# Optimization experiments

Measured on AMD Instinct MI355X. Metric: run time of the kernel, lower is better.

## Reference

```python
import jax, jax.numpy as jnp
import numpy as np

B, S, D = 4, 2048, 1024
H, DK, DV = 16, 64, 64
FF = 4096
EPS = 1e-6


def _ln(x, g, b):
    mu = jnp.mean(x, axis=-1, keepdims=True)
    var = jnp.mean((x - mu) ** 2, axis=-1, keepdims=True)
    return (x - mu) * jax.lax.rsqrt(var + EPS) * g + b


def setup_inputs() -> dict:
    key = jax.random.key(0)
    ks = jax.random.split(key, 12)
    sd = 0.02
    return {
        "src": jax.random.normal(ks[0], (B, S, D), jnp.float32),
        "attn_mask": jnp.zeros((B, S, S), jnp.bool_),
        "Wq": jax.random.normal(ks[1], (D, H * DK), jnp.float32) * sd,
        "bq": jnp.zeros((H * DK,), jnp.float32),
        "Wk": jax.random.normal(ks[2], (D, H * DK), jnp.float32) * sd,
        "bk": jnp.zeros((H * DK,), jnp.float32),
        "Wv": jax.random.normal(ks[3], (D, H * DV), jnp.float32) * sd,
        "bv": jnp.zeros((H * DV,), jnp.float32),
        "Wo": jax.random.normal(ks[4], (D, D), jnp.float32) * sd,
        "bo": jnp.zeros((D,), jnp.float32),
        "ln1_g": jnp.ones((D,), jnp.float32),
        "ln1_b": jnp.zeros((D,), jnp.float32),
        "W1": jax.random.normal(ks[5], (D, FF), jnp.float32) * sd,
        "b1": jnp.zeros((FF,), jnp.float32),
        "W2": jax.random.normal(ks[6], (FF, D), jnp.float32) * sd,
        "b2": jnp.zeros((D,), jnp.float32),
        "ln2_g": jnp.ones((D,), jnp.float32),
        "ln2_b": jnp.zeros((D,), jnp.float32),
    }


def reference(src, attn_mask, Wq, bq, Wk, bk, Wv, bv, Wo, bo,
              ln1_g, ln1_b, W1, b1, W2, b2, ln2_g, ln2_b):
    # QKV projections, split heads: [B,S,H*dk] -> [B,H,S,dk]
    q = (src @ Wq + bq).reshape(B, S, H, DK).transpose(0, 2, 1, 3)
    k = (src @ Wk + bk).reshape(B, S, H, DK).transpose(0, 2, 1, 3)
    v = (src @ Wv + bv).reshape(B, S, H, DV).transpose(0, 2, 1, 3)

    scale = 1.0 / (DK ** 0.5)
    scores = jnp.einsum("bhqd,bhkd->bhqk", q, k) * scale
    scores = jnp.where(attn_mask[:, None, :, :], -1e9, scores)
    attn = jax.nn.softmax(scores, axis=-1)  # dropout = identity (eval)
    ctx = jnp.einsum("bhqk,bhkd->bhqd", attn, v)
    ctx = ctx.transpose(0, 2, 1, 3).reshape(B, S, D)

    att_out = ctx @ Wo + bo  # dropout = identity (eval)
    x = _ln(src + att_out, ln1_g, ln1_b)

    h = jax.nn.relu(x @ W1 + b1)  # dropout = identity (eval)
    ffn_out = h @ W2 + b2
    return _ln(ffn_out + x, ln2_g, ln2_b)
```

## Files before the change

kernel.cpp:

```cpp
#include <hip/hip_runtime.h>
#include <stdint.h>

#define BB 4
#define SS 2048
#define DMODEL 1024
#define NH 16
#define FF 4096
#define MROWS (BB*SS)

typedef __bf16 bf16x8 __attribute__((ext_vector_type(8)));
typedef __bf16 bf16x2t __attribute__((ext_vector_type(2)));
typedef float f32x4 __attribute__((ext_vector_type(4)));
typedef float f32x16 __attribute__((ext_vector_type(16)));
typedef unsigned uintx4 __attribute__((ext_vector_type(4)));

__device__ __forceinline__ unsigned short f2b(float f) {
  unsigned u = __float_as_uint(f);
  unsigned r = (u + 0x7FFFu + ((u >> 16) & 1u)) >> 16;
  return (unsigned short)r;
}

__device__ __forceinline__ unsigned pack2bf(float a, float b) {
  bf16x2t v = {(__bf16)a, (__bf16)b};
  return __builtin_bit_cast(unsigned, v);
}

__device__ __forceinline__ void pls32(unsigned& x, unsigned& y) {
#if defined(__has_builtin) && __has_builtin(__builtin_amdgcn_permlane32_swap)
  auto r = __builtin_amdgcn_permlane32_swap(x, y, 0, 0);
  x = (unsigned)r[0];
  y = (unsigned)r[1];
#else
  const unsigned sx = (unsigned)__shfl_xor((int)x, 32, 64);
  const unsigned sy = (unsigned)__shfl_xor((int)y, 32, 64);
  const bool hi = ((threadIdx.x >> 5) & 1) != 0;
  const unsigned nx = hi ? sy : x;
  const unsigned ny = hi ? y : sx;
  x = nx; y = ny;
#endif
}

__device__ __forceinline__ void gload_lds16(const void* g, void* l) {
  __builtin_amdgcn_global_load_lds(
      (const __attribute__((address_space(1))) void*)g,
      (__attribute__((address_space(3))) void*)l, 16, 0, 0);
}

__device__ __forceinline__ bf16x8 lds_frag(const unsigned short* base, int row, int k) {
  unsigned off = (unsigned)((row * 128 + k * 2) ^ ((row & 7) << 4));
  return *reinterpret_cast<const bf16x8*>(reinterpret_cast<const char*>(base) + off);
}

__device__ __forceinline__ bf16x8 frag_rot(const unsigned short* base, int row, int kElem) {
  const int cb = kElem * 2;
  const unsigned off = (unsigned)(row * 128 + ((((cb >> 4) + row) & 7) << 4) + (cb & 15));
  return *reinterpret_cast<const bf16x8*>(reinterpret_cast<const char*>(base) + off);
}

__global__ __launch_bounds__(256) void f32_to_bf16_k(const float* __restrict__ in,
                                                     unsigned short* __restrict__ out, int n8) {
  const int i = blockIdx.x * 256 + threadIdx.x;
  if (i >= n8) return;
  const float4* p = reinterpret_cast<const float4*>(in) + (size_t)i * 2;
  const float4 a = p[0], c = p[1];
  uint4 o;
  o.x = (unsigned)f2b(a.x) | ((unsigned)f2b(a.y) << 16);
  o.y = (unsigned)f2b(a.z) | ((unsigned)f2b(a.w) << 16);
  o.z = (unsigned)f2b(c.x) | ((unsigned)f2b(c.y) << 16);
  o.w = (unsigned)f2b(c.z) | ((unsigned)f2b(c.w) << 16);
  reinterpret_cast<uint4*>(out)[i] = o;
}

__global__ __launch_bounds__(256) void transpose_convert4_k(
    const float* __restrict__ i0, const float* __restrict__ i1,
    const float* __restrict__ i2, const float* __restrict__ i3,
    unsigned short* __restrict__ o0, unsigned short* __restrict__ o1,
    unsigned short* __restrict__ o2, unsigned short* __restrict__ o3) {
  __shared__ float tile[32][33];
  const int z = blockIdx.z;
  const float* in = (z == 0) ? i0 : (z == 1) ? i1 : (z == 2) ? i2 : i3;
  unsigned short* out = (z == 0) ? o0 : (z == 1) ? o1 : (z == 2) ? o2 : o3;
  const int c0 = blockIdx.x * 32, r0 = blockIdx.y * 32;
  const int tx = threadIdx.x, ty = threadIdx.y;
  #pragma unroll
  for (int i = 0; i < 4; ++i)
    tile[ty + i * 8][tx] = in[(size_t)(r0 + ty + i * 8) * 1024 + c0 + tx];
  __syncthreads();
  #pragma unroll
  for (int i = 0; i < 4; ++i)
    out[(size_t)(c0 + ty + i * 8) * 1024 + r0 + tx] = f2b(tile[tx][ty + i * 8]);
}

__global__ __launch_bounds__(256) void transpose_convert_k(const float* __restrict__ in,
                                                           unsigned short* __restrict__ out,
                                                           int R, int C) {
  __shared__ float tile[32][33];
  const int c0 = blockIdx.x * 32, r0 = blockIdx.y * 32;
  const int tx = threadIdx.x, ty = threadIdx.y;
  #pragma unroll
  for (int i = 0; i < 4; ++i)
    tile[ty + i * 8][tx] = in[(size_t)(r0 + ty + i * 8) * C + c0 + tx];
  __syncthreads();
  #pragma unroll
  for (int i = 0; i < 4; ++i)
    out[(size_t)(c0 + ty + i * 8) * R + r0 + tx] = f2b(tile[tx][ty + i * 8]);
}

__global__ __launch_bounds__(256) void v_transpose_k(const unsigned short* __restrict__ Vb,
                                                     unsigned short* __restrict__ Vt) {
  __shared__ unsigned short tile[32][33];
  const int bh = blockIdx.z, b = bh >> 4, h = bh & 15;
  const int s0 = blockIdx.x * 32, d0 = blockIdx.y * 32;
  const int tx = threadIdx.x, ty = threadIdx.y;
  #pragma unroll
  for (int i = 0; i < 4; ++i)
    tile[ty + i * 8][tx] = Vb[(size_t)(b * SS + s0 + ty + i * 8) * DMODEL + h * 64 + d0 + tx];
  __syncthreads();
  #pragma unroll
  for (int i = 0; i < 4; ++i)
    Vt[(size_t)(bh * 64 + d0 + ty + i * 8) * SS + s0 + tx] = tile[tx][ty + i * 8];
}

__global__ __launch_bounds__(256) void mask_pack_k(const unsigned char* __restrict__ mask,
                                                   unsigned long long* __restrict__ mbits, int total) {
  const int idx = blockIdx.x * 256 + threadIdx.x;
  if (idx >= total) return;
  const uint4* p = reinterpret_cast<const uint4*>(mask) + (size_t)idx * 4;
  unsigned long long bits = 0ull;
  #pragma unroll
  for (int q = 0; q < 4; ++q) {
    uint4 v = p[q];
    unsigned wds[4] = {v.x, v.y, v.z, v.w};
    #pragma unroll
    for (int j = 0; j < 4; ++j)
      #pragma unroll
      for (int by = 0; by < 4; ++by)
        if ((wds[j] >> (by * 8)) & 0xFFu) bits |= 1ull << (q * 16 + j * 4 + by);
  }
  mbits[idx] = bits;
}

#define CQ 0.18033688011112042f
template <int EPI>
__global__ __launch_bounds__(256, 2) void gemm2_k(const unsigned short* __restrict__ A,
                                                  const unsigned short* __restrict__ Bt,
                                                  const float* __restrict__ bias_a,
                                                  const float* __restrict__ bias_b,
                                                  const float* __restrict__ bias_c,
                                                  void* __restrict__ Cout, int N, int K) {
  __shared__ __align__(16) unsigned short As[2][128 * 64];
  __shared__ __align__(16) unsigned short Bs[2][128 * 64];
  const int t = threadIdx.x;
  const int lane = t & 63, w = t >> 6;
  const int wr = w >> 1, wc = w & 1;
  const int lr = lane & 15, lg = lane >> 4;

  const int nwg = gridDim.x;
  const int q8 = nwg >> 3;
  const int wg = (blockIdx.x & 7) * q8 + (blockIdx.x >> 3);
  const int mb = wg & 63, nb = wg >> 6;
  const int m0 = mb * 128, n0 = nb * 128;

  const int srow = t >> 3;
  const unsigned cxor = (unsigned)(((t & 7) * 16) ^ (((t >> 3) & 7) << 4));
  const char* Asrc = reinterpret_cast<const char*>(A) + ((size_t)(m0 + srow) * K) * 2 + cxor;
  const char* Bsrc = reinterpret_cast<const char*>(Bt) + ((size_t)(n0 + srow) * K) * 2 + cxor;
  const size_t rstep = (size_t)32 * K * 2;
  char* AsB[2] = {reinterpret_cast<char*>(As[0]) + w * 1024, reinterpret_cast<char*>(As[1]) + w * 1024};
  char* BsB[2] = {reinterpret_cast<char*>(Bs[0]) + w * 1024, reinterpret_cast<char*>(Bs[1]) + w * 1024};

  auto stage = [&](int buf, int kt) {
    const char* ak = Asrc + (size_t)kt * 128;
    const char* bk = Bsrc + (size_t)kt * 128;
    #pragma unroll
    for (int c = 0; c < 4; ++c) {
      gload_lds16(ak + c * rstep, AsB[buf] + c * 4096);
      gload_lds16(bk + c * rstep, BsB[buf] + c * 4096);
    }
  };

  f32x4 acc[4][4] = {};
  const int nt = K >> 6;

  stage(0, 0);
  stage(1, 1);
  asm volatile("s_waitcnt vmcnt(8)" ::: "memory");
  __builtin_amdgcn_s_barrier();

  int cur = 0;
  for (int kt = 0; kt < nt; ++kt) {
    bf16x8 af[2][4], bfr[2][4];
    #pragma unroll
    for (int kk = 0; kk < 2; ++kk) {
      #pragma unroll
      for (int m = 0; m < 4; ++m)
        af[kk][m] = lds_frag(As[cur], wr * 64 + m * 16 + lr, kk * 32 + lg * 8);
      #pragma unroll
      for (int n = 0; n < 4; ++n)
        bfr[kk][n] = lds_frag(Bs[cur], wc * 64 + n * 16 + lr, kk * 32 + lg * 8);
    }
    __builtin_amdgcn_s_setprio(1);
    #pragma unroll
    for (int m = 0; m < 4; ++m)
      #pragma unroll
      for (int n = 0; n < 4; ++n)
        acc[m][n] = __builtin_amdgcn_mfma_f32_16x16x32_bf16(af[0][m], bfr[0][n], acc[m][n], 0, 0, 0);
    __builtin_amdgcn_s_setprio(0);

    asm volatile("s_waitcnt lgkmcnt(0)" ::: "memory");
    __builtin_amdgcn_s_barrier();
    if (kt + 2 < nt) {
      stage(cur, kt + 2);
      asm volatile("s_waitcnt vmcnt(8)" ::: "memory");
    } else {
      asm volatile("s_waitcnt vmcnt(0)" ::: "memory");
    }
    __builtin_amdgcn_s_barrier();
    __builtin_amdgcn_sched_barrier(0);

    __builtin_amdgcn_s_setprio(1);
    #pragma unroll
    for (int m = 0; m < 4; ++m)
      #pragma unroll
      for (int n = 0; n < 4; ++n)
        acc[m][n] = __builtin_amdgcn_mfma_f32_16x16x32_bf16(af[1][m], bfr[1][n], acc[m][n], 0, 0, 0);
    __builtin_amdgcn_s_setprio(0);
    cur ^= 1;
  }

  const int ccol0 = wc * 64;
  if constexpr (EPI == 3) {
    const int g3 = n0 >> 10;
    const float* bias = (g3 == 0) ? bias_a : (g3 == 1) ? bias_b : bias_c;
    const float scl = (g3 == 0) ? CQ : 1.0f;
    unsigned short* Og = reinterpret_cast<unsigned short*>(Cout) + (size_t)g3 * MROWS * DMODEL;
    const int ncol0 = (n0 & 1023) + ccol0;
    float bv[4];
    #pragma unroll
    for (int n = 0; n < 4; ++n) bv[n] = bias[ncol0 + n * 16 + lr];
    #pragma unroll
    for (int m = 0; m < 4; ++m)
      #pragma unroll
      for (int n = 0; n < 4; ++n)
        #pragma unroll
        for (int i = 0; i < 4; ++i) {
          const float v = (acc[m][n][i] + bv[n]) * scl;
          const size_t row = (size_t)(m0 + wr * 64 + m * 16 + lg * 4 + i);
          Og[row * DMODEL + (ncol0 + n * 16 + lr)] = f2b(v);
        }
  } else {
    float bv[4];
    #pragma unroll
    for (int n = 0; n < 4; ++n) bv[n] = bias_a[n0 + ccol0 + n * 16 + lr];
    #pragma unroll
    for (int m = 0; m < 4; ++m)
      #pragma unroll
      for (int n = 0; n < 4; ++n)
        #pragma unroll
        for (int i = 0; i < 4; ++i) {
          float v = acc[m][n][i] + bv[n];
          if (EPI == 1) v = fmaxf(v, 0.0f);
          const size_t row = (size_t)(m0 + wr * 64 + m * 16 + lg * 4 + i);
          const size_t col = (size_t)(n0 + ccol0 + n * 16 + lr);
          if (EPI == 2) reinterpret_cast<float*>(Cout)[row * N + col] = v;
          else          reinterpret_cast<unsigned short*>(Cout)[row * N + col] = f2b(v);
        }
  }
}

__global__ __launch_bounds__(256) void attn8_k(const unsigned short* __restrict__ Qb,
                                               const unsigned short* __restrict__ Kb,
                                               const unsigned short* __restrict__ Vt,
                                               const unsigned long long* __restrict__ mbits,
                                               unsigned short* __restrict__ ctx) {
  __shared__ __align__(16) unsigned short smem[16384];
  unsigned short* KsC = smem;
  unsigned short* KsN = smem + 4096;
  unsigned short* VsC = smem + 8192;
  unsigned short* VsN = smem + 12288;

  const int t = threadIdx.x;
  const int lane = t & 63, w = t >> 6;
  const int lo = lane & 31, hi = lane >> 5;

  const int flat = blockIdx.x;
  const int bid = (flat & 7) * 128 + (flat >> 3);
  const int bh = bid >> 4, qb = bid & 15;
  const int b = bh >> 4, h = bh & 15;
  const int q0 = qb * 128 + w * 32;

  bf16x8 qf[4];
  {
    const unsigned short* qp = Qb + (size_t)(b * SS + q0 + lo) * DMODEL + h * 64 + hi * 8;
    #pragma unroll
    for (int ds = 0; ds < 4; ++ds) qf[ds] = *reinterpret_cast<const bf16x8*>(qp + ds * 16);
  }

  const uintx4 onesw = {0x3F803F80u, 0x3F803F80u, 0x3F803F80u, 0x3F803F80u};
  const bf16x8 ones = __builtin_bit_cast(bf16x8, onesw);

  f32x16 ao0 = {}, ao1 = {}, dacc = {};

  const int srow = t >> 3;
  const int gsw = ((t & 7) - srow) & 7;
  const char* Ksrc = reinterpret_cast<const char*>(Kb) +
                     ((size_t)(b * SS + srow) * DMODEL + h * 64 + gsw * 8) * 2;
  const char* Vsrc = reinterpret_cast<const char*>(Vt) +
                     ((size_t)(bh * 64 + srow) * SS + gsw * 8) * 2;
  const unsigned wdo = (unsigned)(w * 1024);

  auto stage = [&](int kv, unsigned short* Kbuf, unsigned short* Vbuf) {
    const char* ks0 = Ksrc + (size_t)kv * (64 * DMODEL * 2);
    const char* vs0 = Vsrc + (size_t)kv * 128;
    char* kd = reinterpret_cast<char*>(Kbuf) + wdo;
    char* vd = reinterpret_cast<char*>(Vbuf) + wdo;
    gload_lds16(ks0, kd);
    gload_lds16(ks0 + (size_t)32 * DMODEL * 2, kd + 4096);
    gload_lds16(vs0, vd);
    gload_lds16(vs0 + (size_t)32 * SS * 2, vd + 4096);
  };

  const unsigned long long* mrow = mbits + (size_t)(b * SS + q0 + lo) * (SS / 64);

  stage(0, KsC, VsC);
  asm volatile("s_waitcnt vmcnt(0)" ::: "memory");
  __syncthreads();

  for (int kv = 0; kv < SS / 64; ++kv) {
    if (kv + 1 < SS / 64) stage(kv + 1, KsN, VsN);

    const unsigned long long mb = mrow[kv];

    f32x16 st0 = {}, st1 = {};
    __builtin_amdgcn_s_setprio(1);
    #pragma unroll
    for (int ds = 0; ds < 4; ++ds) {
      const int kcol = ds * 16 + hi * 8;
      const bf16x8 k0 = frag_rot(KsC, lo, kcol);
      const bf16x8 k1 = frag_rot(KsC, 32 + lo, kcol);
      st0 = __builtin_amdgcn_mfma_f32_32x32x16_bf16(k0, qf[ds], st0, 0, 0, 0);
      st1 = __builtin_amdgcn_mfma_f32_32x32x16_bf16(k1, qf[ds], st1, 0, 0, 0);
    }
    __builtin_amdgcn_s_setprio(0);

    if (__any(mb != 0ull)) {
      #pragma unroll
      for (int r = 0; r < 16; ++r) {
        const int k = (r & 3) + 8 * (r >> 2) + 4 * hi;
        if ((mb >> k) & 1ull) st0[r] = -20.0f;
        if ((mb >> (k + 32)) & 1ull) st1[r] = -20.0f;
      }
    }

    #pragma unroll
    for (int r = 0; r < 16; ++r) {
      st0[r] = exp2f(st0[r]);
      st1[r] = exp2f(st1[r]);
    }

    unsigned pw[16];
    #define PACK8(SV, KB)                                            \
      {                                                              \
        unsigned c0 = pack2bf(SV[0], SV[1]);                         \
        unsigned c1 = pack2bf(SV[2], SV[3]);                         \
        unsigned c2 = pack2bf(SV[4], SV[5]);                         \
        unsigned c3 = pack2bf(SV[6], SV[7]);                         \
        unsigned c4 = pack2bf(SV[8], SV[9]);                         \
        unsigned c5 = pack2bf(SV[10], SV[11]);                       \
        unsigned c6 = pack2bf(SV[12], SV[13]);                       \
        unsigned c7 = pack2bf(SV[14], SV[15]);                       \
        pls32(c0, c2); pls32(c1, c3); pls32(c4, c6); pls32(c5, c7);  \
        pw[(KB) + 0] = c0; pw[(KB) + 1] = c1;                        \
        pw[(KB) + 2] = c2; pw[(KB) + 3] = c3;                        \
        pw[(KB) + 4] = c4; pw[(KB) + 5] = c5;                        \
        pw[(KB) + 6] = c6; pw[(KB) + 7] = c7;                        \
      }
    PACK8(st0, 0)
    PACK8(st1, 8)
    #undef PACK8

    __builtin_amdgcn_s_setprio(1);
    #pragma unroll
    for (int ks = 0; ks < 4; ++ks) {
      const uintx4 pv = {pw[ks * 4 + 0], pw[ks * 4 + 1], pw[ks * 4 + 2], pw[ks * 4 + 3]};
      const bf16x8 pb = __builtin_bit_cast(bf16x8, pv);
      const int scol = ks * 16 + hi * 8;
      ao0 = __builtin_amdgcn_mfma_f32_32x32x16_bf16(frag_rot(VsC, lo, scol), pb, ao0, 0, 0, 0);
      ao1 = __builtin_amdgcn_mfma_f32_32x32x16_bf16(frag_rot(VsC, 32 + lo, scol), pb, ao1, 0, 0, 0);
      dacc = __builtin_amdgcn_mfma_f32_32x32x16_bf16(ones, pb, dacc, 0, 0, 0);
    }
    __builtin_amdgcn_s_setprio(0);

    asm volatile("s_waitcnt vmcnt(0)" ::: "memory");
    __syncthreads();
    unsigned short* tk = KsC; KsC = KsN; KsN = tk;
    unsigned short* tv = VsC; VsC = VsN; VsN = tv;
  }

  const float inv = 1.0f / dacc[0];
  unsigned short* Ob = smem + w * 2048;
  #pragma unroll
  for (int dt = 0; dt < 2; ++dt) {
    #pragma unroll
    for (int r = 0; r < 16; ++r) {
      const int d = dt * 32 + (r & 3) + 8 * (r >> 2) + 4 * hi;
      const float v = (dt ? ao1[r] : ao0[r]) * inv;
      const unsigned off = (unsigned)((lo * 128 + d * 2) ^ ((lo & 7) << 4));
      *reinterpret_cast<unsigned short*>(reinterpret_cast<char*>(Ob) + off) = f2b(v);
    }
  }
  __syncthreads();
  const int rr = lane >> 1, xh = (lane & 1) * 64;
  char* crow_g = reinterpret_cast<char*>(ctx) +
                 ((size_t)(b * SS + q0 + rr) * DMODEL + h * 64) * 2;
  #pragma unroll
  for (int c = 0; c < 4; ++c) {
    const unsigned off = (unsigned)((rr * 128 + xh + c * 16) ^ ((rr & 7) << 4));
    const uint4 vv = *reinterpret_cast<const uint4*>(reinterpret_cast<const char*>(Ob) + off);
    *reinterpret_cast<uint4*>(crow_g + xh + c * 16) = vv;
  }
}

__global__ __launch_bounds__(256) void ln_k(const float* __restrict__ a,
                                            const float* __restrict__ res,
                                            const float* __restrict__ g,
                                            const float* __restrict__ be,
                                            float* __restrict__ of,
                                            unsigned short* __restrict__ ob) {
  const int row = blockIdx.x, t = threadIdx.x;
  float4 v = reinterpret_cast<const float4*>(a + (size_t)row * DMODEL)[t];
  const float4 r = reinterpret_cast<const float4*>(res + (size_t)row * DMODEL)[t];
  v.x += r.x; v.y += r.y; v.z += r.z; v.w += r.w;
  float s = v.x + v.y + v.z + v.w;
  float ss = v.x * v.x + v.y * v.y + v.z * v.z + v.w * v.w;
  #pragma unroll
  for (int off = 1; off < 64; off <<= 1) {
    s += __shfl_xor(s, off, 64);
    ss += __shfl_xor(ss, off, 64);
  }
  __shared__ float red[8];
  const int wv = t >> 6;
  if ((t & 63) == 0) { red[wv] = s; red[4 + wv] = ss; }
  __syncthreads();
  s = red[0] + red[1] + red[2] + red[3];
  ss = red[4] + red[5] + red[6] + red[7];
  const float mu = s * (1.0f / DMODEL);
  const float rs = rsqrtf(ss * (1.0f / DMODEL) - mu * mu + 1e-6f);
  const float4 gg = reinterpret_cast<const float4*>(g)[t];
  const float4 bb = reinterpret_cast<const float4*>(be)[t];
  float4 o;
  o.x = (v.x - mu) * rs * gg.x + bb.x;
  o.y = (v.y - mu) * rs * gg.y + bb.y;
  o.z = (v.z - mu) * rs * gg.z + bb.z;
  o.w = (v.w - mu) * rs * gg.w + bb.w;
  if (of) reinterpret_cast<float4*>(of + (size_t)row * DMODEL)[t] = o;
  if (ob) {
    ushort4 u;
    u.x = f2b(o.x); u.y = f2b(o.y); u.z = f2b(o.z); u.w = f2b(o.w);
    reinterpret_cast<ushort4*>(ob + (size_t)row * DMODEL)[t] = u;
  }
}

extern "C" void kernel_launch(void* const* d_in, const int* in_sizes, int n_in,
                              void* d_out, int out_size, void* d_ws, size_t ws_size,
                              hipStream_t stream) {
  const float* src = (const float*)d_in[0];
  const unsigned char* mask = (const unsigned char*)d_in[1];
  const float* Wq = (const float*)d_in[2];
  const float* bq = (const float*)d_in[3];
  const float* Wk = (const float*)d_in[4];
  const float* bk = (const float*)d_in[5];
  const float* Wv = (const float*)d_in[6];
  const float* bv = (const float*)d_in[7];
  const float* Wo = (const float*)d_in[8];
  const float* bo = (const float*)d_in[9];
  const float* ln1_g = (const float*)d_in[10];
  const float* ln1_b = (const float*)d_in[11];
  const float* W1 = (const float*)d_in[12];
  const float* b1 = (const float*)d_in[13];
  const float* W2 = (const float*)d_in[14];
  const float* b2 = (const float*)d_in[15];
  const float* ln2_g = (const float*)d_in[16];
  const float* ln2_b = (const float*)d_in[17];

  char* ws = (char*)d_ws;
  size_t off = 0;
  auto alloc = [&](size_t bytes) {
    char* p = ws + off;
    off += (bytes + 255) & ~(size_t)255;
    return p;
  };
  unsigned short* srcb = (unsigned short*)alloc((size_t)MROWS * DMODEL * 2);
  unsigned short* WqT  = (unsigned short*)alloc((size_t)DMODEL * DMODEL * 2);
  unsigned short* WkT  = (unsigned short*)alloc((size_t)DMODEL * DMODEL * 2);
  unsigned short* WvT  = (unsigned short*)alloc((size_t)DMODEL * DMODEL * 2);
  unsigned short* WoT  = (unsigned short*)alloc((size_t)DMODEL * DMODEL * 2);
  unsigned short* W1T  = (unsigned short*)alloc((size_t)FF * DMODEL * 2);
  unsigned short* W2T  = (unsigned short*)alloc((size_t)DMODEL * FF * 2);
  unsigned short* Qb   = (unsigned short*)alloc((size_t)MROWS * DMODEL * 2);
  unsigned short* Kb   = (unsigned short*)alloc((size_t)MROWS * DMODEL * 2);
  unsigned short* Vb   = (unsigned short*)alloc((size_t)MROWS * DMODEL * 2);
  unsigned short* Vt   = (unsigned short*)alloc((size_t)MROWS * DMODEL * 2);
  unsigned short* ctx  = (unsigned short*)alloc((size_t)MROWS * DMODEL * 2);
  float*          xf   = (float*)alloc((size_t)MROWS * DMODEL * 4);
  unsigned short* xb   = (unsigned short*)alloc((size_t)MROWS * DMODEL * 2);
  unsigned short* hb   = (unsigned short*)alloc((size_t)MROWS * FF * 2);
  unsigned long long* mbits = (unsigned long long*)alloc((size_t)BB * SS * (SS / 64) * 8);
  float* outf = (float*)d_out;
  (void)Kb; (void)Vb;

  f32_to_bf16_k<<<(MROWS * DMODEL / 8 + 255) / 256, 256, 0, stream>>>(src, srcb, MROWS * DMODEL / 8);
  dim3 tb(32, 8);
  transpose_convert4_k<<<dim3(32, 32, 4), tb, 0, stream>>>(Wq, Wk, Wv, Wo, WqT, WkT, WvT, WoT);
  transpose_convert_k<<<dim3(FF / 32, 32), tb, 0, stream>>>(W1, W1T, DMODEL, FF);
  transpose_convert_k<<<dim3(32, FF / 32), tb, 0, stream>>>(W2, W2T, FF, DMODEL);
  mask_pack_k<<<(BB * SS * (SS / 64) + 255) / 256, 256, 0, stream>>>(mask, mbits, BB * SS * (SS / 64));

  gemm2_k<3><<<dim3(64 * 24), 256, 0, stream>>>(srcb, WqT, bq, bk, bv, Qb, 3072, DMODEL);

  v_transpose_k<<<dim3(SS / 32, 2, BB * NH), tb, 0, stream>>>(Vb, Vt);

  attn8_k<<<dim3((SS / 128) * BB * NH), 256, 0, stream>>>(Qb, Kb, Vt, mbits, ctx);

  gemm2_k<2><<<dim3(64 * 8), 256, 0, stream>>>(ctx, WoT, bo, nullptr, nullptr, outf, DMODEL, DMODEL);

  ln_k<<<MROWS, 256, 0, stream>>>(outf, src, ln1_g, ln1_b, xf, xb);

  gemm2_k<1><<<dim3(64 * 32), 256, 0, stream>>>(xb, W1T, b1, nullptr, nullptr, hb, FF, DMODEL);
  gemm2_k<2><<<dim3(64 * 8), 256, 0, stream>>>(hb, W2T, b2, nullptr, nullptr, outf, DMODEL, FF);

  ln_k<<<MROWS, 256, 0, stream>>>(outf, xf, ln2_g, ln2_b, outf, nullptr);
}
```

Measured before the change: 497.3 us.

## Store GEMM outputs and residual in bf16, swizzle GEMM tile order, drop sched barrier

The Wo and W2 GEMMs now write bf16 instead of fp32, and the LayerNorm kernels read bf16 inputs. The second residual uses the bf16 LN1 output instead of a separate fp32 copy, which cuts intermediate memory traffic. GEMM workgroups are remapped into 4x4 supertiles to improve L2 reuse, and a scheduling barrier is removed. Rounding the pre-LN sums and the residual to bf16 costs some accuracy.

```diff
diff --git a/kernel.cpp b/kernel.cpp
--- a/kernel.cpp
+++ b/kernel.cpp
@@ -18,6 +18,9 @@
   unsigned u = __float_as_uint(f);
   unsigned r = (u + 0x7FFFu + ((u >> 16) & 1u)) >> 16;
   return (unsigned short)r;
+}
+__device__ __forceinline__ float b2f(unsigned short u) {
+  return __uint_as_float((unsigned)u << 16);
 }
 
 __device__ __forceinline__ unsigned pack2bf(float a, float b) {
@@ -158,7 +161,10 @@
   const int nwg = gridDim.x;
   const int q8 = nwg >> 3;
   const int wg = (blockIdx.x & 7) * q8 + (blockIdx.x >> 3);
-  const int mb = wg & 63, nb = wg >> 6;
+  const int sid = wg >> 4, within = wg & 15;
+  const int smb = sid & 15, snb = sid >> 4;
+  const int mb = smb * 4 + (within & 3);
+  const int nb = snb * 4 + (within >> 2);
   const int m0 = mb * 128, n0 = nb * 128;
 
   const int srow = t >> 3;
@@ -216,7 +222,6 @@
       asm volatile("s_waitcnt vmcnt(0)" ::: "memory");
     }
     __builtin_amdgcn_s_barrier();
-    __builtin_amdgcn_sched_barrier(0);
 
     __builtin_amdgcn_s_setprio(1);
     #pragma unroll
@@ -262,8 +267,7 @@
           if (EPI == 1) v = fmaxf(v, 0.0f);
           const size_t row = (size_t)(m0 + wr * 64 + m * 16 + lg * 4 + i);
           const size_t col = (size_t)(n0 + ccol0 + n * 16 + lr);
-          if (EPI == 2) reinterpret_cast<float*>(Cout)[row * N + col] = v;
-          else          reinterpret_cast<unsigned short*>(Cout)[row * N + col] = f2b(v);
+          reinterpret_cast<unsigned short*>(Cout)[row * N + col] = f2b(v);
         }
   }
 }
@@ -421,18 +425,53 @@
   }
 }
 
-__global__ __launch_bounds__(256) void ln_k(const float* __restrict__ a,
-                                            const float* __restrict__ res,
-                                            const float* __restrict__ g,
-                                            const float* __restrict__ be,
-                                            float* __restrict__ of,
-                                            unsigned short* __restrict__ ob) {
+__global__ __launch_bounds__(256) void ln1_k(const unsigned short* __restrict__ a,
+                                             const float* __restrict__ res,
+                                             const float* __restrict__ g,
+                                             const float* __restrict__ be,
+                                             unsigned short* __restrict__ ob) {
   const int row = blockIdx.x, t = threadIdx.x;
-  float4 v = reinterpret_cast<const float4*>(a + (size_t)row * DMODEL)[t];
+  const ushort4 av = reinterpret_cast<const ushort4*>(a + (size_t)row * DMODEL)[t];
   const float4 r = reinterpret_cast<const float4*>(res + (size_t)row * DMODEL)[t];
-  v.x += r.x; v.y += r.y; v.z += r.z; v.w += r.w;
-  float s = v.x + v.y + v.z + v.w;
-  float ss = v.x * v.x + v.y * v.y + v.z * v.z + v.w * v.w;
+  float v0 = b2f(av.x) + r.x, v1 = b2f(av.y) + r.y;
+  float v2 = b2f(av.z) + r.z, v3 = b2f(av.w) + r.w;
+  float s = v0 + v1 + v2 + v3;
+  float ss = v0 * v0 + v1 * v1 + v2 * v2 + v3 * v3;
+  #pragma unroll
+  for (int off = 1; off < 64; off <<= 1) {
+    s += __shfl_xor(s, off, 64);
+    ss += __shfl_xor(ss, off, 64);
+  }
+  __shared__ float red[8];
+  const int wv = t >> 6;
+  if ((t & 63) == 0) { red[wv] = s; red[4 + wv] = ss; }
+  __syncthreads();
+  s = red[0] + red[1] + red[2] + red[3];
+  ss = red[4] + red[5] + red[6] + red[7];
+  const float mu = s * (1.0f / DMODEL);
+  const float rs = rsqrtf(ss * (1.0f / DMODEL) - mu * mu + 1e-6f);
+  const float4 gg = reinterpret_cast<const float4*>(g)[t];
+  const float4 bb = reinterpret_cast<const float4*>(be)[t];
+  ushort4 u;
+  u.x = f2b((v0 - mu) * rs * gg.x + bb.x);
+  u.y = f2b((v1 - mu) * rs * gg.y + bb.y);
+  u.z = f2b((v2 - mu) * rs * gg.z + bb.z);
+  u.w = f2b((v3 - mu) * rs * gg.w + bb.w);
+  reinterpret_cast<ushort4*>(ob + (size_t)row * DMODEL)[t] = u;
+}
+
+__global__ __launch_bounds__(256) void ln2_k(const unsigned short* __restrict__ a,
+                                             const unsigned short* __restrict__ res,
+                                             const float* __restrict__ g,
+                                             const float* __restrict__ be,
+                                             float* __restrict__ of) {
+  const int row = blockIdx.x, t = threadIdx.x;
+  const ushort4 av = reinterpret_cast<const ushort4*>(a + (size_t)row * DMODEL)[t];
+  const ushort4 rv = reinterpret_cast<const ushort4*>(res + (size_t)row * DMODEL)[t];
+  float v0 = b2f(av.x) + b2f(rv.x), v1 = b2f(av.y) + b2f(rv.y);
+  float v2 = b2f(av.z) + b2f(rv.z), v3 = b2f(av.w) + b2f(rv.w);
+  float s = v0 + v1 + v2 + v3;
+  float ss = v0 * v0 + v1 * v1 + v2 * v2 + v3 * v3;
   #pragma unroll
   for (int off = 1; off < 64; off <<= 1) {
     s += __shfl_xor(s, off, 64);
@@ -449,16 +488,11 @@
   const float4 gg = reinterpret_cast<const float4*>(g)[t];
   const float4 bb = reinterpret_cast<const float4*>(be)[t];
   float4 o;
-  o.x = (v.x - mu) * rs * gg.x + bb.x;
-  o.y = (v.y - mu) * rs * gg.y + bb.y;
-  o.z = (v.z - mu) * rs * gg.z + bb.z;
-  o.w = (v.w - mu) * rs * gg.w + bb.w;
-  if (of) reinterpret_cast<float4*>(of + (size_t)row * DMODEL)[t] = o;
-  if (ob) {
-    ushort4 u;
-    u.x = f2b(o.x); u.y = f2b(o.y); u.z = f2b(o.z); u.w = f2b(o.w);
-    reinterpret_cast<ushort4*>(ob + (size_t)row * DMODEL)[t] = u;
-  }
+  o.x = (v0 - mu) * rs * gg.x + bb.x;
+  o.y = (v1 - mu) * rs * gg.y + bb.y;
+  o.z = (v2 - mu) * rs * gg.z + bb.z;
+  o.w = (v3 - mu) * rs * gg.w + bb.w;
+  reinterpret_cast<float4*>(of + (size_t)row * DMODEL)[t] = o;
 }
 
 extern "C" void kernel_launch(void* const* d_in, const int* in_sizes, int n_in,
@@ -502,8 +536,9 @@
   unsigned short* Vb   = (unsigned short*)alloc((size_t)MROWS * DMODEL * 2);
   unsigned short* Vt   = (unsigned short*)alloc((size_t)MROWS * DMODEL * 2);
   unsigned short* ctx  = (unsigned short*)alloc((size_t)MROWS * DMODEL * 2);
-  float*          xf   = (float*)alloc((size_t)MROWS * DMODEL * 4);
+  unsigned short* aob  = (unsigned short*)alloc((size_t)MROWS * DMODEL * 2);
   unsigned short* xb   = (unsigned short*)alloc((size_t)MROWS * DMODEL * 2);
+  unsigned short* fob  = (unsigned short*)alloc((size_t)MROWS * DMODEL * 2);
   unsigned short* hb   = (unsigned short*)alloc((size_t)MROWS * FF * 2);
   unsigned long long* mbits = (unsigned long long*)alloc((size_t)BB * SS * (SS / 64) * 8);
   float* outf = (float*)d_out;
@@ -522,12 +557,12 @@
 
   attn8_k<<<dim3((SS / 128) * BB * NH), 256, 0, stream>>>(Qb, Kb, Vt, mbits, ctx);
 
-  gemm2_k<2><<<dim3(64 * 8), 256, 0, stream>>>(ctx, WoT, bo, nullptr, nullptr, outf, DMODEL, DMODEL);
-
-  ln_k<<<MROWS, 256, 0, stream>>>(outf, src, ln1_g, ln1_b, xf, xb);
+  gemm2_k<0><<<dim3(64 * 8), 256, 0, stream>>>(ctx, WoT, bo, nullptr, nullptr, aob, DMODEL, DMODEL);
+
+  ln1_k<<<MROWS, 256, 0, stream>>>(aob, src, ln1_g, ln1_b, xb);
 
   gemm2_k<1><<<dim3(64 * 32), 256, 0, stream>>>(xb, W1T, b1, nullptr, nullptr, hb, FF, DMODEL);
-  gemm2_k<2><<<dim3(64 * 8), 256, 0, stream>>>(hb, W2T, b2, nullptr, nullptr, outf, DMODEL, FF);
-
-  ln_k<<<MROWS, 256, 0, stream>>>(outf, xf, ln2_g, ln2_b, outf, nullptr);
-}
+  gemm2_k<0><<<dim3(64 * 8), 256, 0, stream>>>(hb, W2T, b2, nullptr, nullptr, fob, DMODEL, FF);
+
+  ln2_k<<<MROWS, 256, 0, stream>>>(fob, xb, ln2_g, ln2_b, outf);
+}
```

Measured after the change: 428.1 us. 1.16x faster.
